# Kernel tuning notes

Measured on AMD Instinct MI355X. Metric: run time of the kernel, lower is better.

Reference implementation:

```python
import jax, jax.numpy as jnp
import numpy as np
from jax import lax

N, M, B = 512, 1024, 1024  # signal dim, atoms, batch (batch==m required by X = W @ Gamma)
POWER_ITER = 100
IHT_ITER = 50


def setup_inputs() -> dict:
    key = jax.random.key(0)
    k1, k2 = jax.random.split(key)
    Y = jax.random.normal(k1, (B, N), dtype=jnp.float32)
    W = jax.random.normal(k2, (N, M), dtype=jnp.float32)
    return {"Y": Y, "W": W, "K": 64}


def power_method(W):
    # 100 iterations of X <- X W^T W / ||.||; returns last pre-normalization norm
    # (approx largest eigenvalue of W^T W), matching PowerMethod in the source.
    X0 = jax.random.normal(jax.random.key(42), (1, W.shape[1]), dtype=W.dtype)

    def body(i, carry):
        X, _ = carry
        X2 = (X @ W.T) @ W          # [1, m]
        nm = jnp.linalg.norm(X2)
        return (X2 / nm, nm)

    _, nm = lax.fori_loop(0, POWER_ITER, body, (X0, jnp.asarray(1.0, W.dtype)))
    return nm


def hard_threshold_k(G, K):
    # keep entries strictly larger (in abs) than the (K+1)-th largest per row
    a = jnp.sort(jnp.abs(G), axis=1)[:, ::-1]   # descending per row
    T = a[:, K][:, None]                          # [B, 1]
    return G * (jnp.abs(G) > T).astype(G.dtype)


def reference(Y, W, K):
    # NormDict: column-normalize the dictionary
    W = W / jnp.linalg.norm(W, axis=0)
    c = power_method(W)
    eta = 1.0 / c
    Yn = jnp.linalg.norm(Y)

    # IHT sparse coding
    Gamma = hard_threshold_k(Y @ (eta * W), K)     # [B, m]
    residual = Gamma @ W.T - Y                      # [B, n]

    def step(carry, _):
        Gamma, residual = carry
        Gamma = hard_threshold_k(Gamma - eta * (residual @ W), K)
        residual = Gamma @ W.T - Y
        return (Gamma, residual), jnp.linalg.norm(residual) / Yn

    (Gamma, residual), norms = lax.scan(step, (Gamma, residual), None, length=IHT_ITER)

    X = W @ Gamma  # [n, m] @ [B, m] -> requires B == m, as in the torch source
    return X, Gamma, norms
```

## Files before the change

### kernel.cpp

```cpp
#include <hip/hip_runtime.h>


#define DEV __device__ __forceinline__

constexpr int Nd = 512;
constexpr int Md = 1024;
constexpr int Bd = 1024;
constexpr int Ksp = 64;
constexpr int IHT = 50;

DEV float wave_reduce_f(float v) {
#pragma unroll
  for (int off = 32; off > 0; off >>= 1) v += __shfl_down(v, off);
  return v;
}
DEV double wave_reduce_d(double v) {
#pragma unroll
  for (int off = 32; off > 0; off >>= 1) v += __shfl_down(v, off);
  return v;
}
DEV float rfl_f(float v) {
  return __uint_as_float(__builtin_amdgcn_readfirstlane(__float_as_uint(v)));
}

__global__ __launch_bounds__(256) void k_colnorm(const float* __restrict__ W,
                                                 float* __restrict__ cnorm,
                                                 double* __restrict__ dacc) {
  if (blockIdx.x == 0 && threadIdx.x < 51) dacc[threadIdx.x] = 0.0;
  int col = blockIdx.x * 256 + threadIdx.x;
  double ss = 0.0;
  for (int i = 0; i < Nd; ++i) {
    float w = W[(size_t)i * Md + col];
    ss = fma((double)w, (double)w, ss);
  }
  cnorm[col] = (float)sqrt(ss);
}

__global__ __launch_bounds__(256) void k_normalize(const float* __restrict__ W,
                                                   const float* __restrict__ cnorm,
                                                   float* __restrict__ Wn) {
  int idx = blockIdx.x * 256 + threadIdx.x;
  Wn[idx] = W[idx] / cnorm[idx & (Md - 1)];
}

template <int BM, int BN, int TN>
DEV void gemm_dev(float* __restrict__ AsB, float* __restrict__ BsB,
                  const float* __restrict__ A, int lda, int ta,
                  const float* __restrict__ B, int ldb, int tb,
                  float* __restrict__ C, int ldc, int Kd, float scale,
                  int bx, int by) {
  constexpr int AE = 32 * BM / 256;
  constexpr int BE = 32 * BN / 256;
  constexpr int AS = BM + 4;
  constexpr int BS = BN + 4;
  const int tid = threadIdx.x;
  const int tx = tid % (BN / TN), ty = tid / (BN / TN);
  const int m0 = by * BM, n0 = bx * BN;
  float ra[AE], rb[BE];
  float acc[4][TN];
#pragma unroll
  for (int i = 0; i < 4; ++i)
#pragma unroll
    for (int j = 0; j < TN; ++j) acc[i][j] = 0.f;

  auto loadA = [&](int k0) {
    if (!ta) {
      const int c = tid & 31, r0 = tid >> 5;
#pragma unroll
      for (int i = 0; i < AE; ++i)
        ra[i] = A[(size_t)(m0 + r0 + i * 8) * lda + (k0 + c)];
    } else {
      const int r = tid % BM, c0 = tid / BM;
#pragma unroll
      for (int i = 0; i < AE; ++i)
        ra[i] = A[(size_t)(k0 + c0 + i * (256 / BM)) * lda + (m0 + r)];
    }
  };
  auto storeA = [&]() {
    if (!ta) {
      const int c = tid & 31, r0 = tid >> 5;
#pragma unroll
      for (int i = 0; i < AE; ++i) AsB[c * AS + r0 + i * 8] = ra[i];
    } else {
      const int r = tid % BM, c0 = tid / BM;
#pragma unroll
      for (int i = 0; i < AE; ++i) AsB[(c0 + i * (256 / BM)) * AS + r] = ra[i];
    }
  };
  auto loadB = [&](int k0) {
    if (!tb) {
      const int c = tid % BN, r0 = tid / BN;
#pragma unroll
      for (int i = 0; i < BE; ++i)
        rb[i] = B[(size_t)(k0 + r0 + i * (256 / BN)) * ldb + (n0 + c)];
    } else {
      const int r = tid & 31, c0 = tid >> 5;
#pragma unroll
      for (int i = 0; i < BE; ++i)
        rb[i] = B[(size_t)(n0 + c0 + i * 8) * ldb + (k0 + r)];
    }
  };
  auto storeB = [&]() {
    if (!tb) {
      const int c = tid % BN, r0 = tid / BN;
#pragma unroll
      for (int i = 0; i < BE; ++i) BsB[(r0 + i * (256 / BN)) * BS + c] = rb[i];
    } else {
      const int r = tid & 31, c0 = tid >> 5;
#pragma unroll
      for (int i = 0; i < BE; ++i) BsB[r * BS + c0 + i * 8] = rb[i];
    }
  };

  loadA(0);
  loadB(0);
  storeA();
  storeB();
  __syncthreads();
  for (int k0 = 0; k0 < Kd; k0 += 32) {
    const bool more = (k0 + 32) < Kd;
    if (more) { loadA(k0 + 32); loadB(k0 + 32); }
#pragma unroll
    for (int kk = 0; kk < 32; ++kk) {
      const float4 a4 = *(const float4*)&AsB[kk * AS + ty * 4];
      const float aa[4] = {a4.x, a4.y, a4.z, a4.w};
      float bb[TN];
      if constexpr (TN == 4) {
        const float4 b4 = *(const float4*)&BsB[kk * BS + tx * 4];
        bb[0] = b4.x; bb[1] = b4.y; bb[2] = b4.z; bb[3] = b4.w;
      } else {
        const float2 b2 = *(const float2*)&BsB[kk * BS + tx * 2];
        bb[0] = b2.x; bb[1] = b2.y;
      }
#pragma unroll
      for (int i = 0; i < 4; ++i)
#pragma unroll
        for (int j = 0; j < TN; ++j) acc[i][j] = fmaf(aa[i], bb[j], acc[i][j]);
    }
    if (more) {
      __syncthreads();
      storeA();
      storeB();
      __syncthreads();
    }
  }
#pragma unroll
  for (int i = 0; i < 4; ++i) {
    if constexpr (TN == 4) {
      float4 o;
      o.x = acc[i][0] * scale; o.y = acc[i][1] * scale;
      o.z = acc[i][2] * scale; o.w = acc[i][3] * scale;
      *(float4*)&C[(size_t)(m0 + ty * 4 + i) * ldc + n0 + tx * 4] = o;
    } else {
      float2 o;
      o.x = acc[i][0] * scale; o.y = acc[i][1] * scale;
      *(float2*)&C[(size_t)(m0 + ty * 4 + i) * ldc + n0 + tx * 2] = o;
    }
  }
}

template <int BM, int BN, int TN>
__global__ __launch_bounds__(256) void k_gemm_t(const float* __restrict__ A, int lda, int ta,
                                                const float* __restrict__ B, int ldb, int tb,
                                                float* __restrict__ C, int ldc, int Kd,
                                                float scale) {
  __shared__ __align__(16) float smem[32 * (BM + 4) + 32 * (BN + 4)];
  gemm_dev<BM, BN, TN>(smem, smem + 32 * (BM + 4), A, lda, ta, B, ldb, tb, C,
                       ldc, Kd, scale, blockIdx.x, blockIdx.y);
}

DEV float erfinv_xla(float x) {
  float w = -log1pf(-x * x);
  float p;
  if (w < 5.0f) {
    w = w - 2.5f;
    p = 2.81022636e-08f;
    p = fmaf(p, w, 3.43273939e-07f);
    p = fmaf(p, w, -3.5233877e-06f);
    p = fmaf(p, w, -4.39150654e-06f);
    p = fmaf(p, w, 0.00021858087f);
    p = fmaf(p, w, -0.00125372503f);
    p = fmaf(p, w, -0.00417768164f);
    p = fmaf(p, w, 0.246640727f);
    p = fmaf(p, w, 1.50140941f);
  } else {
    w = sqrtf(w) - 3.0f;
    p = -0.000200214257f;
    p = fmaf(p, w, 0.000100950558f);
    p = fmaf(p, w, 0.00134934322f);
    p = fmaf(p, w, -0.00367342844f);
    p = fmaf(p, w, 0.00573950773f);
    p = fmaf(p, w, -0.0076224613f);
    p = fmaf(p, w, 0.00943887047f);
    p = fmaf(p, w, 1.00167406f);
    p = fmaf(p, w, 2.83297682f);
  }
  return p * x;
}

#define TF_ROUND(r)                                  \
  {                                                  \
    x0 += x1;                                        \
    x1 = (x1 << (r)) | (x1 >> (32 - (r)));           \
    x1 ^= x0;                                        \
  }

DEV float x0_value(unsigned i, int hi) {
  unsigned x0 = i, x1 = i + 512u;
  const unsigned ks0 = 0u, ks1 = 42u, ks2 = 0x1BD11BDAu ^ 42u;
  x0 += ks0; x1 += ks1;
  TF_ROUND(13) TF_ROUND(15) TF_ROUND(26) TF_ROUND(6)  x0 += ks1; x1 += ks2 + 1u;
  TF_ROUND(17) TF_ROUND(29) TF_ROUND(16) TF_ROUND(24) x0 += ks2; x1 += ks0 + 2u;
  TF_ROUND(13) TF_ROUND(15) TF_ROUND(26) TF_ROUND(6)  x0 += ks0; x1 += ks1 + 3u;
  TF_ROUND(17) TF_ROUND(29) TF_ROUND(16) TF_ROUND(24) x0 += ks1; x1 += ks2 + 4u;
  TF_ROUND(13) TF_ROUND(15) TF_ROUND(26) TF_ROUND(6)  x0 += ks2; x1 += ks0 + 5u;
  const float lo = -0.99999994f;
  const float sqrt2 = 1.41421356237f;
  const unsigned bits = hi ? x1 : x0;
  float f = __uint_as_float((bits >> 9) | 0x3f800000u) - 1.0f;
  float u = fmaxf(lo, f * 2.0f + lo);
  return sqrt2 * erfinv_xla(u);
}

__global__ __launch_bounds__(256) void k_front(
    const float* __restrict__ Wn, const float* __restrict__ Y,
    float* __restrict__ Smat, float* __restrict__ Qm, float* __restrict__ YWm,
    double* __restrict__ dacc, float* __restrict__ vout) {
  __shared__ __align__(16) float smem[4352];
  const int i = blockIdx.x;
  const int t = threadIdx.x;
  if (i < 128) {
    gemm_dev<64, 32, 2>(smem, smem + 32 * 68, Wn, Md, 0, Wn, Md, 1, Smat, Nd,
                        Md, 1.0f, i % 16, i / 16);
  } else if (i < 384) {
    const int j = i - 128;
    gemm_dev<64, 64, 4>(smem, smem + 32 * 68, Wn, Md, 1, Wn, Md, 0, Qm, Md,
                        Nd, 1.0f, j % 16, j / 16);
  } else if (i < 640) {
    const int j = i - 384;
    gemm_dev<64, 64, 4>(smem, smem + 32 * 68, Y, Nd, 0, Wn, Md, 0, YWm, Md,
                        Nd, 1.0f, j % 16, j / 16);
  } else if (i < 768) {
    const int j = i - 640;
    double* red = (double*)smem;
    double s = 0.0;
    for (int idx = j * 256 + t; idx < Bd * Nd; idx += 128 * 256) {
      float y = Y[idx];
      s = fma((double)y, (double)y, s);
    }
    s = wave_reduce_d(s);
    const int lane = t & 63, wid = t >> 6;
    if (lane == 0) red[wid] = s;
    __syncthreads();
    if (t == 0) atomicAdd(&dacc[0], red[0] + red[1] + red[2] + red[3]);
  } else {
    const int j = i - 768;
    float* x0s = smem;
    x0s[t] = x0_value((unsigned)t, 0);
    x0s[t + 512] = x0_value((unsigned)t, 1);
    x0s[t + 256] = x0_value((unsigned)(t + 256), 0);
    x0s[t + 768] = x0_value((unsigned)(t + 256), 1);
    __syncthreads();
    const int lane = t & 63, wid = t >> 6;
    const int row = j * 4 + wid;
    const float4* wr = (const float4*)(Wn + (size_t)row * Md);
    const float4* x4 = (const float4*)x0s;
    float s = 0.f;
#pragma unroll
    for (int e = 0; e < 4; ++e) {
      const float4 w4 = wr[lane + e * 64];
      const float4 xx = x4[lane + e * 64];
      s = fmaf(w4.x, xx.x, s); s = fmaf(w4.y, xx.y, s);
      s = fmaf(w4.z, xx.z, s); s = fmaf(w4.w, xx.w, s);
    }
    s = wave_reduce_f(s);
    if (lane == 0) vout[row] = s;
  }
}

__global__ __launch_bounds__(256) void k_pmv(const float* __restrict__ Mmat,
                                             const float* __restrict__ vin,
                                             float* __restrict__ vout, float scale) {
  const int lane = threadIdx.x & 63, wid = threadIdx.x >> 6;
  const int row = blockIdx.x * 4 + wid;
  const float4* mr = (const float4*)(Mmat + (size_t)row * Nd);
  const float4* v4 = (const float4*)vin;
  float s = 0.f;
#pragma unroll
  for (int e = 0; e < 2; ++e) {
    const float4 m4 = mr[lane + e * 64];
    const float4 xx = v4[lane + e * 64];
    s = fmaf(m4.x, xx.x, s); s = fmaf(m4.y, xx.y, s);
    s = fmaf(m4.z, xx.z, s); s = fmaf(m4.w, xx.w, s);
  }
  s = wave_reduce_f(s);
  if (lane == 0) vout[row] = s * scale;
}

__global__ __launch_bounds__(512) void k_pfinal(const float* __restrict__ v99,
                                                const float* __restrict__ v100,
                                                float* __restrict__ cbuf) {
  __shared__ double r99[8], r100[8];
  const int t = threadIdx.x, lane = t & 63, wid = t >> 6;
  double a = (double)v99[t]; a *= a;
  double b = (double)v100[t]; b *= b;
  a = wave_reduce_d(a);
  b = wave_reduce_d(b);
  if (lane == 0) { r99[wid] = a; r100[wid] = b; }
  __syncthreads();
  if (t == 0) {
    double n99 = 0.0, n100 = 0.0;
    for (int i = 0; i < 8; ++i) { n99 += r99[i]; n100 += r100[i]; }
    float c = (float)(8.0 * sqrt(n100 / n99));
    cbuf[0] = c;
    cbuf[1] = 1.0f / c;
  }
}

__global__ __launch_bounds__(256, 4) void k_iht_all(
    const float* __restrict__ Q, const float* __restrict__ YW,
    const float* __restrict__ cbuf, float* __restrict__ gdense,
    double* __restrict__ normacc) {
  __shared__ float u[Md];
  __shared__ float yws[Md];
  __shared__ float sval[Ksp];
  __shared__ int sidx[Ksp];
  __shared__ unsigned histbuf[2][4][256];
  __shared__ unsigned wred[4];
  __shared__ unsigned sel_need, sel_prefix;
  __shared__ double dred0;
  __shared__ int scnt;

  const int t = threadIdx.x;
  const int b = blockIdx.x;
  const int lane = t & 63, wv = t >> 6;
  const float eta = cbuf[1];
  const float4 yw = ((const float4*)(YW + (size_t)b * Md))[t];
  ((float4*)yws)[t] = yw;
#pragma unroll
  for (int e = 0; e < 8; ++e) ((unsigned*)histbuf)[t + e * 256] = 0u;
  const float* Qt = Q + t * 4;
  float gdr[4] = {0.f, 0.f, 0.f, 0.f};

  auto scan_select = [&](unsigned(*hist)[256], unsigned pfx, unsigned nd, int sh) {
    const unsigned c0 = hist[0][lane] + hist[1][lane] + hist[2][lane] + hist[3][lane];
    const unsigned c1 = hist[0][lane + 64] + hist[1][lane + 64] + hist[2][lane + 64] + hist[3][lane + 64];
    const unsigned c2 = hist[0][lane + 128] + hist[1][lane + 128] + hist[2][lane + 128] + hist[3][lane + 128];
    const unsigned c3 = hist[0][lane + 192] + hist[1][lane + 192] + hist[2][lane + 192] + hist[3][lane + 192];
    unsigned s0 = c0, s1 = c1, s2 = c2, s3 = c3;
#pragma unroll
    for (int off = 1; off < 64; off <<= 1) {
      const unsigned y0 = __shfl_down(s0, off), y1 = __shfl_down(s1, off);
      const unsigned y2 = __shfl_down(s2, off), y3 = __shfl_down(s3, off);
      if (lane + off < 64) { s0 += y0; s1 += y1; s2 += y2; s3 += y3; }
    }
    const unsigned T1 = __builtin_amdgcn_readfirstlane(s1);
    const unsigned T2 = __builtin_amdgcn_readfirstlane(s2);
    const unsigned T3 = __builtin_amdgcn_readfirstlane(s3);
    const unsigned i0 = s0 + T1 + T2 + T3;
    const unsigned i1 = s1 + T2 + T3;
    const unsigned i2 = s2 + T3;
    const unsigned i3 = s3;
    if (i0 >= nd && i0 - c0 < nd) { sel_prefix = pfx | ((unsigned)lane << sh); sel_need = nd - (i0 - c0); }
    if (i1 >= nd && i1 - c1 < nd) { sel_prefix = pfx | ((unsigned)(lane + 64) << sh); sel_need = nd - (i1 - c1); }
    if (i2 >= nd && i2 - c2 < nd) { sel_prefix = pfx | ((unsigned)(lane + 128) << sh); sel_need = nd - (i2 - c2); }
    if (i3 >= nd && i3 - c3 < nd) { sel_prefix = pfx | ((unsigned)(lane + 192) << sh); sel_need = nd - (i3 - c3); }
  };

  for (int it = -1; it < IHT; ++it) {
    float vals[4];
    unsigned key[4];
    int cnt = 0;
    if (it >= 0) {
      cnt = scnt;
      float4 p = make_float4(0.f, 0.f, 0.f, 0.f);
      float4 qa[8], qb[8];
      float ga[8], gb[8];
      auto LOAD8 = [&](float4* q, float* g, int kk) {
#pragma unroll
        for (int j = 0; j < 8; ++j) {
          const int id = __builtin_amdgcn_readfirstlane(sidx[kk + j]);
          g[j] = rfl_f(sval[kk + j]);
          q[j] = *(const float4*)(Qt + (size_t)id * Md);
        }
      };
      auto FMA8 = [&](const float4* q, const float* g) {
#pragma unroll
        for (int j = 0; j < 8; ++j) p.x = fmaf(g[j], q[j].x, p.x);
#pragma unroll
        for (int j = 0; j < 8; ++j) p.y = fmaf(g[j], q[j].y, p.y);
#pragma unroll
        for (int j = 0; j < 8; ++j) p.z = fmaf(g[j], q[j].z, p.z);
#pragma unroll
        for (int j = 0; j < 8; ++j) p.w = fmaf(g[j], q[j].w, p.w);
      };
      int k = 0;
      const int nfull = cnt & ~7;
      if (nfull >= 8) {
        LOAD8(qa, ga, 0);
        k = 8;
        for (; k + 16 <= nfull; k += 16) {
          LOAD8(qb, gb, k);
          FMA8(qa, ga);
          LOAD8(qa, ga, k + 8);
          FMA8(qb, gb);
        }
        if (k + 8 <= nfull) {
          LOAD8(qb, gb, k);
          FMA8(qa, ga);
          FMA8(qb, gb);
          k += 8;
        } else {
          FMA8(qa, ga);
        }
      }
      for (; k < cnt; ++k) {
        const int id = __builtin_amdgcn_readfirstlane(sidx[k]);
        const float g = rfl_f(sval[k]);
        const float4 q = *(const float4*)(Qt + (size_t)id * Md);
        p.x = fmaf(g, q.x, p.x); p.y = fmaf(g, q.y, p.y);
        p.z = fmaf(g, q.z, p.z); p.w = fmaf(g, q.w, p.w);
      }
      ((float4*)u)[t] = p;
      vals[0] = -(eta * (p.x - yw.x)) + gdr[0];
      vals[1] = -(eta * (p.y - yw.y)) + gdr[1];
      vals[2] = -(eta * (p.z - yw.z)) + gdr[2];
      vals[3] = -(eta * (p.w - yw.w)) + gdr[3];
    } else {
      vals[0] = eta * yw.x; vals[1] = eta * yw.y;
      vals[2] = eta * yw.z; vals[3] = eta * yw.w;
      __syncthreads();
    }
#pragma unroll
    for (int e = 0; e < 4; ++e) key[e] = __float_as_uint(vals[e]) & 0x7fffffffu;

#pragma unroll
    for (int e = 0; e < 4; ++e) atomicAdd(&histbuf[1][wv][key[e] >> 24], 1u);
    __syncthreads();
    if (wv == 0) {
      scan_select(histbuf[1], 0u, Ksp + 1, 24);
    } else if (wv == 1) {
      if (it >= 1) {
        double part = 0.0;
        if (lane < cnt) {
          const int id = sidx[lane];
          part = (double)sval[lane] * ((double)u[id] - 2.0 * (double)yws[id]);
        }
        part = wave_reduce_d(part);
        if (lane == 0) dred0 = part;
      }
    } else {
      unsigned* hz = (unsigned*)histbuf[0] + (wv - 2) * 512;
#pragma unroll
      for (int e = 0; e < 8; ++e) hz[lane + e * 64] = 0u;
    }
    __syncthreads();
    unsigned prefix = sel_prefix;
    unsigned need = sel_need;
    unsigned pmask = 0xFF000000u;

#pragma unroll
    for (int pass = 2; pass >= 0; --pass) {
      const int sh = 8 * pass;
      const int pb = pass & 1;
      unsigned(*hist)[256] = histbuf[pb];
#pragma unroll
      for (int e = 0; e < 4; ++e)
        if ((key[e] & pmask) == prefix) atomicAdd(&hist[wv][(key[e] >> sh) & 255u], 1u);
      if (pass == 2 && it >= 1 && t == 0) atomicAdd(&normacc[it - 1], dred0);
      __syncthreads();
      unsigned* hz = histbuf[pb ^ 1][wv];
      hz[lane] = 0u; hz[lane + 64] = 0u; hz[lane + 128] = 0u; hz[lane + 192] = 0u;
      if (wv == 0) scan_select(hist, prefix, need, sh);
      __syncthreads();
      prefix = sel_prefix;
      need = sel_need;
      pmask |= (255u << sh);
    }
    const unsigned Tbits = prefix;

    unsigned keep = 0u;
    unsigned myc = 0u;
#pragma unroll
    for (int e = 0; e < 4; ++e)
      if (key[e] > Tbits) { keep |= (1u << e); ++myc; }
    gdr[0] = (keep & 1u) ? vals[0] : 0.f;
    gdr[1] = (keep & 2u) ? vals[1] : 0.f;
    gdr[2] = (keep & 4u) ? vals[2] : 0.f;
    gdr[3] = (keep & 8u) ? vals[3] : 0.f;
    unsigned x = myc;
#pragma unroll
    for (int off = 1; off < 64; off <<= 1) {
      const unsigned y = __shfl_up(x, off);
      if (lane >= off) x += y;
    }
    if (lane == 63) wred[wv] = x;
    __syncthreads();
    unsigned addlo = 0u;
    for (int w2 = 0; w2 < wv; ++w2) addlo += wred[w2];
    int base = (int)(x + addlo) - (int)myc;
#pragma unroll
    for (int e = 0; e < 4; ++e) {
      if (keep & (1u << e)) {
        sidx[base] = t * 4 + e;
        sval[base] = vals[e];
        ++base;
      }
    }
    if (t == 0) scnt = (int)(wred[0] + wred[1] + wred[2] + wred[3]);
    if (it == IHT - 1) {
      float4 g;
      g.x = gdr[0]; g.y = gdr[1]; g.z = gdr[2]; g.w = gdr[3];
      ((float4*)(gdense + (size_t)b * Md))[t] = g;
    }
    __syncthreads();
  }

  const int cnt = scnt;
  if (wv == 0) {
    double part = 0.0;
    if (lane < cnt) {
      const int id = sidx[lane];
      float acc2 = 0.f;
      for (int k = 0; k < cnt; ++k)
        acc2 = fmaf(sval[k], Q[(size_t)sidx[k] * Md + id], acc2);
      part = (double)sval[lane] * ((double)acc2 - 2.0 * (double)yws[id]);
    }
    part = wave_reduce_d(part);
    if (lane == 0) atomicAdd(&normacc[IHT - 1], part);
  }
}

__global__ __launch_bounds__(256) void k_back(
    const float* __restrict__ Wn, const float* __restrict__ G,
    float* __restrict__ X, const double* __restrict__ dacc,
    float* __restrict__ onorms) {
  __shared__ __align__(16) float smem[4352];
  const int i = blockIdx.x;
  if (i < 256) {
    gemm_dev<64, 32, 2>(smem, smem + 32 * 68, Wn, Md, 0, G, Md, 0, X, Md, Md,
                        1.0f, i % 32, i / 32);
  } else {
    const int t = threadIdx.x;
    if (t < IHT) {
      const double yn2 = dacc[0];
      double r2 = yn2 + dacc[1 + t];
      if (r2 < 0.0) r2 = 0.0;
      onorms[t] = (float)(sqrt(r2) / sqrt(yn2));
    }
  }
}

extern "C" void kernel_launch(void* const* d_in, const int* in_sizes, int n_in,
                              void* d_out, int out_size, void* d_ws, size_t ws_size,
                              hipStream_t stream) {
  (void)in_sizes; (void)n_in; (void)out_size; (void)ws_size;
  const float* Y = (const float*)d_in[0];
  const float* W = (const float*)d_in[1];
  float* out = (float*)d_out;
  float* outX = out;
  float* outG = out + Nd * Md;
  float* outN = outG + Bd * Md;

  char* wsb = (char*)d_ws;
  double* dacc = (double*)wsb;
  float* cbuf = (float*)(wsb + 512);
  float* Wn = (float*)(wsb + 1024);
  float* Q = Wn + Nd * Md;
  float* YW = Q + Md * Md;
  float* Smat = YW + Bd * Md;
  float* S2 = Smat + Nd * Nd;
  float* cnorm = S2 + Nd * Nd;
  float* X0 = cnorm + Md;
  float* V = X0 + Md;

  k_colnorm<<<4, 256, 0, stream>>>(W, cnorm, dacc);
  k_normalize<<<2048, 256, 0, stream>>>(W, cnorm, Wn);

  k_front<<<896, 256, 0, stream>>>(Wn, Y, Smat, Q, YW, dacc, V);

  k_gemm_t<64, 32, 2><<<dim3(16, 8), 256, 0, stream>>>(Smat, Nd, 0, Smat, Nd, 0, S2, Nd, Nd, 0.015625f);

  float* pin = V;
  float* pout = V + 512;
  for (int i = 0; i < 49; ++i) {
    k_pmv<<<128, 256, 0, stream>>>(S2, pin, pout, 1.0f);
    float* tp = pin; pin = pout; pout = tp;
  }
  k_pmv<<<128, 256, 0, stream>>>(Smat, pin, V + 1024, 0.125f);
  k_pmv<<<128, 256, 0, stream>>>(Smat, V + 1024, V + 1536, 0.125f);
  k_pfinal<<<1, 512, 0, stream>>>(V + 1024, V + 1536, cbuf);

  k_iht_all<<<1024, 256, 0, stream>>>(Q, YW, cbuf, outG, dacc + 1);

  k_back<<<257, 256, 0, stream>>>(Wn, outG, outX, dacc, outN);
}
```

Measured before the change: 878.1 us.

## Chain power-iteration matvecs in few launches with inter-block atomic counters

Replaces 51 separate matrix-vector kernel launches with 7 launches, each covering up to 8 dependent steps. Blocks of later steps spin on a global atomic counter until all 128 blocks of the previous step have released their results. The input vector is staged in shared memory. This cuts per-launch overhead, at the cost of relying on blocks being scheduled in order, since a later step's block could otherwise occupy a CU while waiting on an earlier one that has not run.

```diff
diff --git a/kernel.cpp b/kernel.cpp
--- a/kernel.cpp
+++ b/kernel.cpp
@@ -22,11 +22,21 @@
 DEV float rfl_f(float v) {
   return __uint_as_float(__builtin_amdgcn_readfirstlane(__float_as_uint(v)));
 }
+DEV float vload_f(const float* p) {
+  return __hip_atomic_load(p, __ATOMIC_RELAXED, __HIP_MEMORY_SCOPE_AGENT);
+}
+DEV void vstore_f(float* p, float v) {
+  __hip_atomic_store(p, v, __ATOMIC_RELAXED, __HIP_MEMORY_SCOPE_AGENT);
+}
 
 __global__ __launch_bounds__(256) void k_colnorm(const float* __restrict__ W,
                                                  float* __restrict__ cnorm,
-                                                 double* __restrict__ dacc) {
-  if (blockIdx.x == 0 && threadIdx.x < 51) dacc[threadIdx.x] = 0.0;
+                                                 double* __restrict__ dacc,
+                                                 unsigned* __restrict__ pcnt) {
+  if (blockIdx.x == 0) {
+    if (threadIdx.x < 51) dacc[threadIdx.x] = 0.0;
+    if (threadIdx.x >= 64 && threadIdx.x < 128) pcnt[threadIdx.x - 64] = 0u;
+  }
   int col = blockIdx.x * 256 + threadIdx.x;
   double ss = 0.0;
   for (int i = 0; i < Nd; ++i) {
@@ -278,13 +288,33 @@
   }
 }
 
-__global__ __launch_bounds__(256) void k_pmv(const float* __restrict__ Mmat,
-                                             const float* __restrict__ vin,
-                                             float* __restrict__ vout, float scale) {
-  const int lane = threadIdx.x & 63, wid = threadIdx.x >> 6;
-  const int row = blockIdx.x * 4 + wid;
-  const float4* mr = (const float4*)(Mmat + (size_t)row * Nd);
-  const float4* v4 = (const float4*)vin;
+__global__ __launch_bounds__(256, 4) void k_pchain(
+    const float* __restrict__ S2m, const float* __restrict__ Smat,
+    float* __restrict__ vbase, unsigned* __restrict__ cnt, int gbase) {
+  __shared__ __align__(16) float vin_s[Nd];
+  const int t = threadIdx.x, lane = t & 63, wid = t >> 6;
+  const int st = blockIdx.x >> 7;
+  const int idx = blockIdx.x & 127;
+  const int g = gbase + st;
+  if (st > 0) {
+    if (t == 0) {
+      while (__hip_atomic_load(&cnt[g - 1], __ATOMIC_ACQUIRE,
+                               __HIP_MEMORY_SCOPE_AGENT) < 128u)
+        __builtin_amdgcn_s_sleep(8);
+    }
+    __syncthreads();
+  }
+  const float* src = vbase + ((g <= 49) ? ((g & 1) * Nd) : (2 * Nd));
+  float* dst = vbase + ((g <= 48) ? (((g + 1) & 1) * Nd)
+                                  : ((g == 49) ? 2 * Nd : 3 * Nd));
+  const float* M = (g < 49) ? S2m : Smat;
+  const float scale = (g < 49) ? 1.0f : 0.125f;
+  vin_s[t] = vload_f(&src[t]);
+  vin_s[t + 256] = vload_f(&src[t + 256]);
+  __syncthreads();
+  const int row = idx * 4 + wid;
+  const float4* mr = (const float4*)(M + (size_t)row * Nd);
+  const float4* v4 = (const float4*)vin_s;
   float s = 0.f;
 #pragma unroll
   for (int e = 0; e < 2; ++e) {
@@ -294,7 +324,11 @@
     s = fmaf(m4.z, xx.z, s); s = fmaf(m4.w, xx.w, s);
   }
   s = wave_reduce_f(s);
-  if (lane == 0) vout[row] = s * scale;
+  if (lane == 0) vstore_f(&dst[row], s * scale);
+  __syncthreads();
+  if (t == 0)
+    __hip_atomic_fetch_add(&cnt[g], 1u, __ATOMIC_RELEASE,
+                           __HIP_MEMORY_SCOPE_AGENT);
 }
 
 __global__ __launch_bounds__(512) void k_pfinal(const float* __restrict__ v99,
@@ -573,22 +607,19 @@
   float* cnorm = S2 + Nd * Nd;
   float* X0 = cnorm + Md;
   float* V = X0 + Md;
-
-  k_colnorm<<<4, 256, 0, stream>>>(W, cnorm, dacc);
+  unsigned* pcnt = (unsigned*)(V + 2048);
+
+  k_colnorm<<<4, 256, 0, stream>>>(W, cnorm, dacc, pcnt);
   k_normalize<<<2048, 256, 0, stream>>>(W, cnorm, Wn);
 
   k_front<<<896, 256, 0, stream>>>(Wn, Y, Smat, Q, YW, dacc, V);
 
   k_gemm_t<64, 32, 2><<<dim3(16, 8), 256, 0, stream>>>(Smat, Nd, 0, Smat, Nd, 0, S2, Nd, Nd, 0.015625f);
 
-  float* pin = V;
-  float* pout = V + 512;
-  for (int i = 0; i < 49; ++i) {
-    k_pmv<<<128, 256, 0, stream>>>(S2, pin, pout, 1.0f);
-    float* tp = pin; pin = pout; pout = tp;
-  }
-  k_pmv<<<128, 256, 0, stream>>>(Smat, pin, V + 1024, 0.125f);
-  k_pmv<<<128, 256, 0, stream>>>(Smat, V + 1024, V + 1536, 0.125f);
+  for (int l = 0; l < 51; l += 8) {
+    const int ns = (51 - l < 8) ? (51 - l) : 8;
+    k_pchain<<<ns * 128, 256, 0, stream>>>(S2, Smat, V, pcnt, l);
+  }
   k_pfinal<<<1, 512, 0, stream>>>(V + 1024, V + 1536, cbuf);
 
   k_iht_all<<<1024, 256, 0, stream>>>(Q, YW, cbuf, outG, dacc + 1);
```

Measured after the change: 2.177 ms. +147.9%, slower.
